# Optimization experiments

Hardware: AMD Instinct MI355X
Metric: run time of the kernel (lower is better)

Reference implementation:

```python
import jax, jax.numpy as jnp
import numpy as np

D = 1024      # d_model
H = 16        # nhead
HD = D // H   # head_dim = 64
R = HD        # rotary_dim (default = head_dim)
N, T = 2, 2048
W_LEFT, W_RIGHT = 127, 128  # attn_window
ROPE_BASE = 10000.0


def _rope(x, cos, sin):
    # x: [N, T, H, HD]; cos/sin: [1, T, 1, R//2]; non-interleaved (rotate-half)
    x1 = x[..., : R // 2]
    x2 = x[..., R // 2 : R]
    rot = jnp.concatenate([x1 * cos - x2 * sin, x2 * cos + x1 * sin], axis=-1)
    if R < x.shape[-1]:
        rot = jnp.concatenate([rot, x[..., R:]], axis=-1)
    return rot


def setup_inputs() -> dict:
    key = jax.random.key(0)
    k1, k2, k3, k4 = jax.random.split(key, 4)
    x = jax.random.normal(k1, (N, T, D), dtype=jnp.float32)
    w_qkv = jax.random.normal(k2, (3 * D, D), dtype=jnp.float32) * 0.02
    w_out = jax.random.normal(k3, (D, D), dtype=jnp.float32) * 0.02
    b_out = jax.random.normal(k4, (D,), dtype=jnp.float32) * 0.02
    return {"x": x, "w_qkv": w_qkv, "w_out": w_out, "b_out": b_out}


def reference(x, w_qkv, w_out, b_out):
    n, t, _ = x.shape
    qkv = (x @ w_qkv.T).reshape(n, t, 3, H, HD)
    q, k, v = qkv[:, :, 0], qkv[:, :, 1], qkv[:, :, 2]  # [N, T, H, HD]

    # Rotary embedding (flash-attn RotaryEmbedding, interleaved=False)
    pos = jnp.arange(t, dtype=jnp.float32)
    inv_freq = 1.0 / (ROPE_BASE ** (jnp.arange(0, R, 2, dtype=jnp.float32) / R))
    freqs = pos[:, None] * inv_freq[None, :]          # [T, R//2]
    cos = jnp.cos(freqs)[None, :, None, :]
    sin = jnp.sin(freqs)[None, :, None, :]
    q = _rope(q, cos, sin)
    k = _rope(k, cos, sin)

    # Sliding-window band mask: keep j in [i - W_LEFT, i + W_RIGHT]
    i = jnp.arange(t)[:, None]
    j = jnp.arange(t)[None, :]
    band = (j >= i - W_LEFT) & (j <= i + W_RIGHT)      # [T, T] bool
    bias = jnp.where(band, 0.0, -jnp.inf).astype(x.dtype)

    scale = np.float32(1.0 / np.sqrt(HD))
    scores = jnp.einsum('nthd,nshd->nhts', q, k) * scale + bias  # [N, H, T, T]
    probs = jax.nn.softmax(scores, axis=-1)
    attn = jnp.einsum('nhts,nshd->nthd', probs, v).reshape(n, t, D)
    return attn @ w_out.T + b_out
```

## Files before the change

### kernel.cpp

```cpp
#include <hip/hip_runtime.h>
#include <math.h>

#define D_MODEL 1024
#define N_HEADS 16
#define HEAD_DIM 64
#define BATCH 2
#define SEQ 2048
#define WIN_L 127
#define WIN_R 128

typedef float f32x4 __attribute__((ext_vector_type(4)));
typedef __bf16 bf16x8 __attribute__((ext_vector_type(8)));
typedef unsigned short ushort8_t __attribute__((ext_vector_type(8)));

typedef const __attribute__((address_space(1))) void* gptr_t;
typedef __attribute__((address_space(3))) void* lptr_t;

__device__ __forceinline__ unsigned short f2bf(float v) {
    unsigned u = __float_as_uint(v);
    unsigned r = (u + 0x7FFF + ((u >> 16) & 1)) >> 16;
    return (unsigned short)r;
}

#define NX_ELEM (4096 * 1024)
#define NW_ELEM (3072 * 1024)
#define NO_ELEM (1024 * 1024)

__global__ __launch_bounds__(256)
void cvt_all(const float* __restrict__ x, const float* __restrict__ wq,
             const float* __restrict__ wo, unsigned short* __restrict__ xb,
             unsigned short* __restrict__ wqb, unsigned short* __restrict__ wob)
{
    int i = (blockIdx.x * 256 + threadIdx.x) * 4;
    const float* src;
    unsigned short* dst;
    int off;
    if (i < NX_ELEM)                 { src = x;  dst = xb;  off = i; }
    else if (i < NX_ELEM + NW_ELEM)  { src = wq; dst = wqb; off = i - NX_ELEM; }
    else                             { src = wo; dst = wob; off = i - NX_ELEM - NW_ELEM; }
    float4 f = *(const float4*)(src + off);
    ushort4 o;
    o.x = f2bf(f.x); o.y = f2bf(f.y); o.z = f2bf(f.z); o.w = f2bf(f.w);
    *(ushort4*)(dst + off) = o;
}

__global__ __launch_bounds__(256, 3)
void gemm_qkv(const unsigned short* __restrict__ A,
              const unsigned short* __restrict__ B,
              unsigned short* __restrict__ qb,
              unsigned short* __restrict__ kb,
              unsigned short* __restrict__ vbT,
              int M, int N, int K)
{
    __shared__ __attribute__((aligned(16))) unsigned short U[17408];
    unsigned short* Al0 = U;
    unsigned short* Bl0 = U + 4096;
    unsigned short* Al1 = U + 8192;
    unsigned short* Bl1 = U + 12288;

    const int tid  = threadIdx.x;
    const int wave = tid >> 6;
    const int lane = tid & 63;
    const int m0 = blockIdx.y * 128;
    const int n0 = blockIdx.x * 128;

    const int wm = (wave >> 1) * 64;
    const int wn = (wave & 1) * 64;
    const int quad = lane >> 4;
    const int l16  = lane & 15;

    const int srow = lane >> 2;
    const int scol = (lane & 3) * 8;

    f32x4 acc[4][4] = {};

    for (int k0 = 0; k0 < K; k0 += 64) {
        __syncthreads();
#pragma unroll
        for (int l = 0; l < 2; ++l) {
            const int r = l * 64 + wave * 16 + srow;
            const unsigned short* gA = A + (size_t)(m0 + r) * K + k0 + scol;
            const unsigned short* gB = B + (size_t)(n0 + r) * K + k0 + scol;
            __builtin_amdgcn_global_load_lds((gptr_t)gA,        (lptr_t)&Al0[r * 32 + scol], 16, 0, 0);
            __builtin_amdgcn_global_load_lds((gptr_t)gB,        (lptr_t)&Bl0[r * 32 + scol], 16, 0, 0);
            __builtin_amdgcn_global_load_lds((gptr_t)(gA + 32), (lptr_t)&Al1[r * 32 + scol], 16, 0, 0);
            __builtin_amdgcn_global_load_lds((gptr_t)(gB + 32), (lptr_t)&Bl1[r * 32 + scol], 16, 0, 0);
        }
        __syncthreads();

#pragma unroll
        for (int kh = 0; kh < 2; ++kh) {
            const unsigned short* Ap = kh ? Al1 : Al0;
            const unsigned short* Bp = kh ? Bl1 : Bl0;
            bf16x8 af[4], bf[4];
#pragma unroll
            for (int i = 0; i < 4; ++i)
                af[i] = *(const bf16x8*)&Ap[(wm + i * 16 + l16) * 32 + quad * 8];
#pragma unroll
            for (int j = 0; j < 4; ++j)
                bf[j] = *(const bf16x8*)&Bp[(wn + j * 16 + l16) * 32 + quad * 8];
#pragma unroll
            for (int i = 0; i < 4; ++i)
#pragma unroll
                for (int j = 0; j < 4; ++j)
                    acc[i][j] = __builtin_amdgcn_mfma_f32_16x16x32_bf16(af[i], bf[j], acc[i][j], 0, 0, 0);
        }
    }

    __syncthreads();

    const int which = (n0 >> 10);
    unsigned short* Tw = U + wave * 4352;

    if (which != 2) {
        float invf[2];
#pragma unroll
        for (int jp = 0; jp < 2; ++jp)
            invf[jp] = exp2f(-(float)(jp * 16 + l16) * 0.41524101186092f);
#pragma unroll
        for (int i = 0; i < 4; ++i) {
            const int tb = (m0 + wm + i * 16 + quad * 4) & 2047;
#pragma unroll
            for (int jp = 0; jp < 2; ++jp)
#pragma unroll
                for (int r = 0; r < 4; ++r) {
                    float s, c;
                    __sincosf((float)(tb + r) * invf[jp], &s, &c);
                    float x1 = acc[i][jp][r], x2 = acc[i][jp + 2][r];
                    acc[i][jp][r]     = x1 * c - x2 * s;
                    acc[i][jp + 2][r] = x2 * c + x1 * s;
                }
        }
#pragma unroll
        for (int i = 0; i < 4; ++i)
#pragma unroll
            for (int j = 0; j < 4; ++j)
#pragma unroll
                for (int r = 0; r < 4; ++r)
                    Tw[(i * 16 + quad * 4 + r) * 68 + j * 16 + l16] = f2bf(acc[i][j][r]);
    } else {
#pragma unroll
        for (int i = 0; i < 4; ++i)
#pragma unroll
            for (int j = 0; j < 4; ++j) {
                ushort4 pv;
                pv.x = f2bf(acc[i][j][0]); pv.y = f2bf(acc[i][j][1]);
                pv.z = f2bf(acc[i][j][2]); pv.w = f2bf(acc[i][j][3]);
                *(ushort4*)&Tw[(j * 16 + l16) * 68 + i * 16 + quad * 4] = pv;
            }
    }

    {
        const int h   = ((n0 + wn) >> 6) & 15;
        const int nb  = (m0 + wm) >> 11;
        const int tw0 = (m0 + wm) & 2047;
        const int lr8 = lane >> 3;
        const int lc8 = (lane & 7) * 8;
        if (which != 2) {
            unsigned short* dst = (which == 0 ? qb : kb);
            unsigned short* gb = dst + (((size_t)nb * 16 + h) * SEQ + tw0) * 64;
#pragma unroll
            for (int c = 0; c < 8; ++c) {
                const int row = c * 8 + lr8;
                ushort4 lo = *(const ushort4*)&Tw[row * 68 + lc8];
                ushort4 hi = *(const ushort4*)&Tw[row * 68 + lc8 + 4];
                ushort8_t v8 = {lo.x, lo.y, lo.z, lo.w, hi.x, hi.y, hi.z, hi.w};
                *(ushort8_t*)&gb[row * 64 + lc8] = v8;
            }
        } else {
            unsigned short* gb = vbT + ((size_t)nb * 16 + h) * 64 * SEQ + tw0;
#pragma unroll
            for (int c = 0; c < 8; ++c) {
                const int drow = c * 8 + lr8;
                ushort4 lo = *(const ushort4*)&Tw[drow * 68 + lc8];
                ushort4 hi = *(const ushort4*)&Tw[drow * 68 + lc8 + 4];
                ushort8_t v8 = {lo.x, lo.y, lo.z, lo.w, hi.x, hi.y, hi.z, hi.w};
                *(ushort8_t*)&gb[(size_t)drow * SEQ + lc8] = v8;
            }
        }
    }
}

__global__ __launch_bounds__(256, 4)
void gemm_out(const unsigned short* __restrict__ A,
              const unsigned short* __restrict__ B,
              const float* __restrict__ bias, float* __restrict__ C,
              int M, int N, int K)
{
    __shared__ __attribute__((aligned(16))) unsigned short Al0[64 * 32];
    __shared__ __attribute__((aligned(16))) unsigned short Al1[64 * 32];
    __shared__ __attribute__((aligned(16))) unsigned short Bl0[128 * 32];
    __shared__ __attribute__((aligned(16))) unsigned short Bl1[128 * 32];

    const int tid  = threadIdx.x;
    const int wave = tid >> 6;
    const int lane = tid & 63;
    const int m0 = blockIdx.y * 64;
    const int n0 = blockIdx.x * 128;

    const int wm = (wave >> 1) * 32;
    const int wn = (wave & 1) * 64;
    const int quad = lane >> 4;
    const int l16  = lane & 15;

    const int srow = lane >> 2;
    const int scol = (lane & 3) * 8;

    f32x4 acc[2][4] = {};

    for (int k0 = 0; k0 < K; k0 += 64) {
        __syncthreads();
        {
            const int r = wave * 16 + srow;
            const unsigned short* gA = A + (size_t)(m0 + r) * K + k0 + scol;
            __builtin_amdgcn_global_load_lds((gptr_t)gA,        (lptr_t)&Al0[r * 32 + scol], 16, 0, 0);
            __builtin_amdgcn_global_load_lds((gptr_t)(gA + 32), (lptr_t)&Al1[r * 32 + scol], 16, 0, 0);
#pragma unroll
            for (int l = 0; l < 2; ++l) {
                const int rb = l * 64 + wave * 16 + srow;
                const unsigned short* gB = B + (size_t)(n0 + rb) * K + k0 + scol;
                __builtin_amdgcn_global_load_lds((gptr_t)gB,        (lptr_t)&Bl0[rb * 32 + scol], 16, 0, 0);
                __builtin_amdgcn_global_load_lds((gptr_t)(gB + 32), (lptr_t)&Bl1[rb * 32 + scol], 16, 0, 0);
            }
        }
        __syncthreads();

#pragma unroll
        for (int kh = 0; kh < 2; ++kh) {
            const unsigned short* Ap = kh ? Al1 : Al0;
            const unsigned short* Bp = kh ? Bl1 : Bl0;
            bf16x8 af[2], bf[4];
#pragma unroll
            for (int i = 0; i < 2; ++i)
                af[i] = *(const bf16x8*)&Ap[(wm + i * 16 + l16) * 32 + quad * 8];
#pragma unroll
            for (int j = 0; j < 4; ++j)
                bf[j] = *(const bf16x8*)&Bp[(wn + j * 16 + l16) * 32 + quad * 8];
#pragma unroll
            for (int i = 0; i < 2; ++i)
#pragma unroll
                for (int j = 0; j < 4; ++j)
                    acc[i][j] = __builtin_amdgcn_mfma_f32_16x16x32_bf16(af[i], bf[j], acc[i][j], 0, 0, 0);
        }
    }

#pragma unroll
    for (int i = 0; i < 2; ++i) {
        const int row_base = m0 + wm + i * 16 + quad * 4;
#pragma unroll
        for (int j = 0; j < 4; ++j) {
            const int col = n0 + wn + j * 16 + l16;
            const float bv = bias[col];
#pragma unroll
            for (int r = 0; r < 4; ++r)
                C[(size_t)(row_base + r) * N + col] = acc[i][j][r] + bv;
        }
    }
}

__global__ __launch_bounds__(256, 4)
void attn_mfma(const unsigned short* __restrict__ qb,
               const unsigned short* __restrict__ kb,
               const unsigned short* __restrict__ vbT,
               unsigned short* __restrict__ attnb)
{
    __shared__ unsigned short Pl[4][16][296];

    const int tid  = threadIdx.x;
    const int w    = tid >> 6;
    const int lane = tid & 63;
    const int quad = lane >> 4;
    const int l16  = lane & 15;

    const int t0 = blockIdx.x * 64;
    const int h  = blockIdx.y;
    const int nB = blockIdx.z;
    const int nh = nB * 16 + h;

    const int tw  = t0 + w * 16;
    const int klo = max(0, tw - WIN_L) & ~31;
    const int khi = min(SEQ, tw + 16 + WIN_R);
    const int nchunk = (khi - klo + 31) >> 5;

    const unsigned short* qrow = qb + ((size_t)nh * SEQ + tw + l16) * 64;
    bf16x8 aq0 = *(const bf16x8*)(qrow + quad * 8);
    bf16x8 aq1 = *(const bf16x8*)(qrow + 32 + quad * 8);

    const unsigned short* kbase = kb + (size_t)nh * SEQ * 64;
    const unsigned short* vbase = vbT + (size_t)nh * 64 * SEQ;

    const int trow = tw + quad * 4;
    const int keyc = l16;

    f32x4 oacc[4] = {};
    float sm[4] = {0.f, 0.f, 0.f, 0.f};

    for (int kc = 0; kc < nchunk; ++kc) {
        const int s0 = klo + kc * 32;
        const int kr0 = min(s0 + l16, SEQ - 1);
        const int kr1 = min(s0 + 16 + l16, SEQ - 1);
        const unsigned short* kp0 = kbase + (size_t)kr0 * 64;
        const unsigned short* kp1 = kbase + (size_t)kr1 * 64;
        bf16x8 bk00 = *(const bf16x8*)(kp0 + quad * 8);
        bf16x8 bk01 = *(const bf16x8*)(kp0 + 32 + quad * 8);
        bf16x8 bk10 = *(const bf16x8*)(kp1 + quad * 8);
        bf16x8 bk11 = *(const bf16x8*)(kp1 + 32 + quad * 8);
        f32x4 sa = {0.f, 0.f, 0.f, 0.f};
        f32x4 sb = {0.f, 0.f, 0.f, 0.f};
        sa = __builtin_amdgcn_mfma_f32_16x16x32_bf16(aq0, bk00, sa, 0, 0, 0);
        sa = __builtin_amdgcn_mfma_f32_16x16x32_bf16(aq1, bk01, sa, 0, 0, 0);
        sb = __builtin_amdgcn_mfma_f32_16x16x32_bf16(aq0, bk10, sb, 0, 0, 0);
        sb = __builtin_amdgcn_mfma_f32_16x16x32_bf16(aq1, bk11, sb, 0, 0, 0);

        const int key0 = s0 + keyc;
        const int key1 = s0 + 16 + keyc;
#pragma unroll
        for (int r = 0; r < 4; ++r) {
            const int t = trow + r;
            const bool v0 = (key0 < khi) && (key0 >= t - WIN_L) && (key0 <= t + WIN_R);
            const bool v1 = (key1 < khi) && (key1 >= t - WIN_L) && (key1 <= t + WIN_R);
            float p0 = v0 ? __expf(sa[r] * 0.125f) : 0.f;
            float p1 = v1 ? __expf(sb[r] * 0.125f) : 0.f;
            sm[r] += p0 + p1;
            Pl[w][quad * 4 + r][kc * 32 + keyc]      = f2bf(p0);
            Pl[w][quad * 4 + r][kc * 32 + 16 + keyc] = f2bf(p1);
        }

        bf16x8 pf = *(const bf16x8*)&Pl[w][l16][kc * 32 + quad * 8];
        const int toff = s0 + quad * 8;
#pragma unroll
        for (int j = 0; j < 4; ++j) {
            bf16x8 vf = *(const bf16x8*)(vbase + (size_t)(j * 16 + l16) * SEQ + toff);
            oacc[j] = __builtin_amdgcn_mfma_f32_16x16x32_bf16(pf, vf, oacc[j], 0, 0, 0);
        }
    }

#pragma unroll
    for (int r = 0; r < 4; ++r) {
#pragma unroll
        for (int o = 8; o >= 1; o >>= 1) sm[r] += __shfl_xor(sm[r], o, 64);
        sm[r] = 1.0f / sm[r];
    }

#pragma unroll
    for (int j = 0; j < 4; ++j)
#pragma unroll
        for (int r = 0; r < 4; ++r) {
            const int t = trow + r;
            attnb[((size_t)(nB * SEQ + t)) * D_MODEL + h * 64 + j * 16 + l16] =
                f2bf(oacc[j][r] * sm[r]);
        }
}

extern "C" void kernel_launch(void* const* d_in, const int* in_sizes, int n_in,
                              void* d_out, int out_size, void* d_ws, size_t ws_size,
                              hipStream_t stream)
{
    (void)in_sizes; (void)n_in; (void)out_size; (void)ws_size;
    const float* x     = (const float*)d_in[0];
    const float* w_qkv = (const float*)d_in[1];
    const float* w_out = (const float*)d_in[2];
    const float* b_out = (const float*)d_in[3];
    float* out = (float*)d_out;

    const int M = BATCH * SEQ;

    unsigned short* qb  = (unsigned short*)d_ws;
    unsigned short* kb  = qb  + (size_t)4194304;
    unsigned short* vbT = kb  + (size_t)4194304;
    unsigned short* wob = vbT + (size_t)4194304;
    unsigned short* xb  = wob + (size_t)1048576;
    unsigned short* wqb = xb  + (size_t)4194304;
    unsigned short* attnb = xb;

    dim3 blk(256);

    cvt_all<<<dim3((NX_ELEM + NW_ELEM + NO_ELEM) / 4 / 256), blk, 0, stream>>>(
        x, w_qkv, w_out, xb, wqb, wob);

    gemm_qkv<<<dim3(3 * D_MODEL / 128, M / 128), blk, 0, stream>>>(
        xb, wqb, qb, kb, vbT, M, 3 * D_MODEL, D_MODEL);

    attn_mfma<<<dim3(SEQ / 64, N_HEADS, BATCH), blk, 0, stream>>>(qb, kb, vbT, attnb);

    gemm_out<<<dim3(D_MODEL / 128, M / 64), blk, 0, stream>>>(
        attnb, wob, b_out, out, M, D_MODEL, D_MODEL);
}
```

Baseline: 169.1 us.

## Stage block's V window in LDS and pack P writes with interleaved keys

Each block now cooperatively loads the full V^T window its four waves need (64 rows by 328 keys) into shared memory once, so the PV MFMA reads V from LDS instead of global memory. Keys are remapped so each lane handles two adjacent keys, which lets a lane write both bf16 probabilities with a single 32-bit LDS store into a smaller per-wave P buffer indexed per chunk. The larger LDS footprint (about 42KB) comes with lowering launch bounds to 3 blocks per CU, which cuts occupancy, and a __syncthreads is added before compute.

```diff
diff --git a/kernel.cpp b/kernel.cpp
--- a/kernel.cpp
+++ b/kernel.cpp
@@ -258,13 +258,14 @@
     }
 }
 
-__global__ __launch_bounds__(256, 4)
+__global__ __launch_bounds__(256, 3)
 void attn_mfma(const unsigned short* __restrict__ qb,
                const unsigned short* __restrict__ kb,
                const unsigned short* __restrict__ vbT,
                unsigned short* __restrict__ attnb)
 {
-    __shared__ unsigned short Pl[4][16][296];
+    __shared__ __attribute__((aligned(16))) unsigned short Vl[64 * 328];
+    __shared__ __attribute__((aligned(16))) unsigned short Pl[4][16 * 40];
 
     const int tid  = threadIdx.x;
     const int w    = tid >> 6;
@@ -277,6 +278,20 @@
     const int nB = blockIdx.z;
     const int nh = nB * 16 + h;
 
+    const int klo_b = max(0, t0 - WIN_L) & ~31;
+
+    {
+        const unsigned short* vbase = vbT + (size_t)nh * 64 * SEQ;
+        for (int s = tid; s < 64 * 41; s += 256) {
+            const int row = s / 41;
+            const int seg = s - row * 41;
+            const int tsrc = min(klo_b + seg * 8, SEQ - 8);
+            ushort8_t v = *(const ushort8_t*)(vbase + (size_t)row * SEQ + tsrc);
+            *(ushort8_t*)&Vl[row * 328 + seg * 8] = v;
+        }
+    }
+    __syncthreads();
+
     const int tw  = t0 + w * 16;
     const int klo = max(0, tw - WIN_L) & ~31;
     const int khi = min(SEQ, tw + 16 + WIN_R);
@@ -287,50 +302,47 @@
     bf16x8 aq1 = *(const bf16x8*)(qrow + 32 + quad * 8);
 
     const unsigned short* kbase = kb + (size_t)nh * SEQ * 64;
-    const unsigned short* vbase = vbT + (size_t)nh * 64 * SEQ;
+    unsigned short* Pw = &Pl[w][0];
 
     const int trow = tw + quad * 4;
-    const int keyc = l16;
 
     f32x4 oacc[4] = {};
     float sm[4] = {0.f, 0.f, 0.f, 0.f};
 
     for (int kc = 0; kc < nchunk; ++kc) {
         const int s0 = klo + kc * 32;
-        const int kr0 = min(s0 + l16, SEQ - 1);
-        const int kr1 = min(s0 + 16 + l16, SEQ - 1);
-        const unsigned short* kp0 = kbase + (size_t)kr0 * 64;
-        const unsigned short* kp1 = kbase + (size_t)kr1 * 64;
-        bf16x8 bk00 = *(const bf16x8*)(kp0 + quad * 8);
-        bf16x8 bk01 = *(const bf16x8*)(kp0 + 32 + quad * 8);
-        bf16x8 bk10 = *(const bf16x8*)(kp1 + quad * 8);
-        bf16x8 bk11 = *(const bf16x8*)(kp1 + 32 + quad * 8);
+        const int keyA = s0 + 2 * l16;
+        const int keyB = keyA + 1;
+        const unsigned short* kpA = kbase + (size_t)min(keyA, SEQ - 1) * 64;
+        const unsigned short* kpB = kbase + (size_t)min(keyB, SEQ - 1) * 64;
+        bf16x8 bkA0 = *(const bf16x8*)(kpA + quad * 8);
+        bf16x8 bkA1 = *(const bf16x8*)(kpA + 32 + quad * 8);
+        bf16x8 bkB0 = *(const bf16x8*)(kpB + quad * 8);
+        bf16x8 bkB1 = *(const bf16x8*)(kpB + 32 + quad * 8);
         f32x4 sa = {0.f, 0.f, 0.f, 0.f};
         f32x4 sb = {0.f, 0.f, 0.f, 0.f};
-        sa = __builtin_amdgcn_mfma_f32_16x16x32_bf16(aq0, bk00, sa, 0, 0, 0);
-        sa = __builtin_amdgcn_mfma_f32_16x16x32_bf16(aq1, bk01, sa, 0, 0, 0);
-        sb = __builtin_amdgcn_mfma_f32_16x16x32_bf16(aq0, bk10, sb, 0, 0, 0);
-        sb = __builtin_amdgcn_mfma_f32_16x16x32_bf16(aq1, bk11, sb, 0, 0, 0);
-
-        const int key0 = s0 + keyc;
-        const int key1 = s0 + 16 + keyc;
+        sa = __builtin_amdgcn_mfma_f32_16x16x32_bf16(aq0, bkA0, sa, 0, 0, 0);
+        sa = __builtin_amdgcn_mfma_f32_16x16x32_bf16(aq1, bkA1, sa, 0, 0, 0);
+        sb = __builtin_amdgcn_mfma_f32_16x16x32_bf16(aq0, bkB0, sb, 0, 0, 0);
+        sb = __builtin_amdgcn_mfma_f32_16x16x32_bf16(aq1, bkB1, sb, 0, 0, 0);
+
 #pragma unroll
         for (int r = 0; r < 4; ++r) {
             const int t = trow + r;
-            const bool v0 = (key0 < khi) && (key0 >= t - WIN_L) && (key0 <= t + WIN_R);
-            const bool v1 = (key1 < khi) && (key1 >= t - WIN_L) && (key1 <= t + WIN_R);
-            float p0 = v0 ? __expf(sa[r] * 0.125f) : 0.f;
-            float p1 = v1 ? __expf(sb[r] * 0.125f) : 0.f;
+            const bool vA = (keyA < khi) && (keyA >= t - WIN_L) && (keyA <= t + WIN_R);
+            const bool vB = (keyB < khi) && (keyB >= t - WIN_L) && (keyB <= t + WIN_R);
+            float p0 = vA ? __expf(sa[r] * 0.125f) : 0.f;
+            float p1 = vB ? __expf(sb[r] * 0.125f) : 0.f;
             sm[r] += p0 + p1;
-            Pl[w][quad * 4 + r][kc * 32 + keyc]      = f2bf(p0);
-            Pl[w][quad * 4 + r][kc * 32 + 16 + keyc] = f2bf(p1);
-        }
-
-        bf16x8 pf = *(const bf16x8*)&Pl[w][l16][kc * 32 + quad * 8];
-        const int toff = s0 + quad * 8;
+            unsigned pk = (unsigned)f2bf(p0) | ((unsigned)f2bf(p1) << 16);
+            *(unsigned*)&Pw[(quad * 4 + r) * 40 + 2 * l16] = pk;
+        }
+
+        bf16x8 pf = *(const bf16x8*)&Pw[l16 * 40 + quad * 8];
+        const int rel = s0 - klo_b + quad * 8;
 #pragma unroll
         for (int j = 0; j < 4; ++j) {
-            bf16x8 vf = *(const bf16x8*)(vbase + (size_t)(j * 16 + l16) * SEQ + toff);
+            bf16x8 vf = *(const bf16x8*)&Vl[(j * 16 + l16) * 328 + rel];
             oacc[j] = __builtin_amdgcn_mfma_f32_16x16x32_bf16(pf, vf, oacc[j], 0, 0, 0);
         }
     }
```

Result: no change. 167.5 us (-0.9%).
